# Performance work log

Hardware: AMD Instinct MI355X
Metric: run time of the kernel (lower is better)

The kernel has to match this reference:

```python
import jax, jax.numpy as jnp
import numpy as np

N = 512        # number of evidences
D = 512        # hidden_dim

def setup_inputs() -> dict:
    key = jax.random.key(0)
    k0, k1, k2, k3, k4 = jax.random.split(key, 5)
    s = 1.0 / np.sqrt(2 * D)
    return {
        "h_e":  jax.random.normal(k0, (N, D), dtype=jnp.float32),
        "W0_w": jax.random.uniform(k1, (D, 2 * D), minval=-s, maxval=s, dtype=jnp.float32),  # nn.Linear(2d, d).weight
        "W0_b": jax.random.uniform(k2, (D,), minval=-s, maxval=s, dtype=jnp.float32),
        "W1_w": jax.random.uniform(k3, (1, D), minval=-1/np.sqrt(D), maxval=1/np.sqrt(D), dtype=jnp.float32),
        "W1_b": jax.random.uniform(k4, (1,), minval=-1/np.sqrt(D), maxval=1/np.sqrt(D), dtype=jnp.float32),
    }

def reference(h_e, W0_w, W0_b, W0b_unused=None, W1_w=None, W1_b=None):
    pass  # placeholder replaced below

def reference(h_e, W0_w, W0_b, W1_w, W1_b):
    d = h_e.shape[-1]
    # W_0([h_i ; h_j]) == h_i @ A^T + h_j @ B^T where W0_w = [A | B]
    Wa = W0_w[:, :d]          # [d, d] acts on h_i
    Wb = W0_w[:, d:]          # [d, d] acts on h_j
    pre_i = jnp.einsum('id,hd->ih', h_e, Wa)            # [n, d]
    pre_j = jnp.einsum('jd,hd->jh', h_e, Wb)            # [n, d]
    hidden = jax.nn.relu(pre_i[:, None, :] + pre_j[None, :, :] + W0_b)  # [n, n, d]
    p = jnp.einsum('ijh,oh->ijo', hidden, W1_w)[..., 0] + W1_b[0]       # [n, n]
    a = jax.nn.softmax(p, axis=-1)                                      # [n, n]
    return a @ h_e                                                      # [n, d]
```

## Files before the change

kernel.cpp:

```cpp
#include <hip/hip_runtime.h>


#define LDS_STRIDE 68

using bf16x8 = __attribute__((ext_vector_type(8))) short;
using f32x4  = __attribute__((ext_vector_type(4))) float;

__device__ __forceinline__ unsigned short f2bf(float x) {
    unsigned int u = __float_as_uint(x);
    u += 0x7fffu + ((u >> 16) & 1u);
    return (unsigned short)(u >> 16);
}

__global__ __launch_bounds__(256) void k_prep(const float* __restrict__ he,
                                              const float* __restrict__ w0,
                                              unsigned short* __restrict__ heb,
                                              unsigned short* __restrict__ hebT,
                                              unsigned short* __restrict__ w0b) {
    const int tid = threadIdx.x;
    if (blockIdx.z == 0) {
        __shared__ unsigned short T[64][65];
        const int r0 = blockIdx.y * 64, c0 = blockIdx.x * 64;
        #pragma unroll
        for (int rep = 0; rep < 4; ++rep) {
            int f = tid + rep * 256;
            int row = f >> 4, col = (f & 15) * 4;
            float4 a = *(const float4*)&he[(r0 + row) * 512 + c0 + col];
            unsigned short q0 = f2bf(a.x), q1 = f2bf(a.y), q2 = f2bf(a.z), q3 = f2bf(a.w);
            *(ushort4*)&heb[(r0 + row) * 512 + c0 + col] = make_ushort4(q0, q1, q2, q3);
            T[row][col + 0] = q0; T[row][col + 1] = q1;
            T[row][col + 2] = q2; T[row][col + 3] = q3;
        }
        __syncthreads();
        #pragma unroll
        for (int rep = 0; rep < 4; ++rep) {
            int f = tid + rep * 256;
            int trow = f >> 4, tcol = (f & 15) * 4;
            ushort4 v = make_ushort4(T[tcol + 0][trow], T[tcol + 1][trow],
                                     T[tcol + 2][trow], T[tcol + 3][trow]);
            *(ushort4*)&hebT[(c0 + trow) * 512 + r0 + tcol] = v;
        }
    } else {
        const int r0 = blockIdx.y * 64, c0 = blockIdx.x * 64 + (blockIdx.z - 1) * 512;
        #pragma unroll
        for (int rep = 0; rep < 4; ++rep) {
            int f = tid + rep * 256;
            int row = f >> 4, col = (f & 15) * 4;
            float4 a = *(const float4*)&w0[(r0 + row) * 1024 + c0 + col];
            *(ushort4*)&w0b[(r0 + row) * 1024 + c0 + col] =
                make_ushort4(f2bf(a.x), f2bf(a.y), f2bf(a.z), f2bf(a.w));
        }
    }
}

__global__ __launch_bounds__(64) void k_preA(const unsigned short* __restrict__ heb,
                                             const unsigned short* __restrict__ w0b,
                                             float* __restrict__ Cfull) {
    const int l = threadIdx.x;
    const int c0 = blockIdx.x * 32;
    const int i0 = blockIdx.y * 32;
    const int r16 = l & 15;
    const int k0l = (l >> 4) * 8;
    const int hrow0 = c0 & 511;
    const int dofs = (c0 >= 512) ? 512 : 0;

    f32x4 acc[2][2] = {};
    const unsigned short* pa0 = heb + (i0 + r16) * 512;
    const unsigned short* pa1 = heb + (i0 + 16 + r16) * 512;
    const unsigned short* pb0 = w0b + (hrow0 + r16) * 1024 + dofs;
    const unsigned short* pb1 = w0b + (hrow0 + 16 + r16) * 1024 + dofs;

    #pragma unroll
    for (int ks = 0; ks < 16; ++ks) {
        const int k0 = ks * 32 + k0l;
        bf16x8 a0 = *(const bf16x8*)(pa0 + k0);
        bf16x8 a1 = *(const bf16x8*)(pa1 + k0);
        bf16x8 b0 = *(const bf16x8*)(pb0 + k0);
        bf16x8 b1 = *(const bf16x8*)(pb1 + k0);
        acc[0][0] = __builtin_amdgcn_mfma_f32_16x16x32_bf16(a0, b0, acc[0][0], 0, 0, 0);
        acc[0][1] = __builtin_amdgcn_mfma_f32_16x16x32_bf16(a0, b1, acc[0][1], 0, 0, 0);
        acc[1][0] = __builtin_amdgcn_mfma_f32_16x16x32_bf16(a1, b0, acc[1][0], 0, 0, 0);
        acc[1][1] = __builtin_amdgcn_mfma_f32_16x16x32_bf16(a1, b1, acc[1][1], 0, 0, 0);
    }
    const int orow = (l >> 4) * 4;
    #pragma unroll
    for (int ti = 0; ti < 2; ++ti)
        #pragma unroll
        for (int tj = 0; tj < 2; ++tj)
            #pragma unroll
            for (int r = 0; r < 4; ++r)
                Cfull[(i0 + ti * 16 + orow + r) * 1024 + c0 + tj * 16 + r16] = acc[ti][tj][r];
}

__global__ __launch_bounds__(256) void k_score(const float* __restrict__ Cfull,
                                               const float* __restrict__ b0,
                                               const float* __restrict__ w1,
                                               float* __restrict__ Ppart) {
    const int tid = threadIdx.x;
    const int tx = tid & 15, ty = tid >> 4;
    const int j0 = blockIdx.x * 64;
    const int i0 = blockIdx.y * 64;
    const int hs = blockIdx.z;

    __shared__ float As[32 * LDS_STRIDE];
    __shared__ float Bs[32 * LDS_STRIDE];
    __shared__ float Ws[32];

    float acc[4][4] = {};

    for (int kt = 0; kt < 2; ++kt) {
        const int hb = hs * 64 + kt * 32;
        #pragma unroll
        for (int r = 0; r < 2; ++r) {
            int f = tid + r * 256;
            int row = f >> 3;
            int hc = (f & 7) * 4;
            float4 a = *(const float4*)&Cfull[(i0 + row) * 1024 + hb + hc];
            As[(hc + 0) * LDS_STRIDE + row] = a.x;
            As[(hc + 1) * LDS_STRIDE + row] = a.y;
            As[(hc + 2) * LDS_STRIDE + row] = a.z;
            As[(hc + 3) * LDS_STRIDE + row] = a.w;
        }
        #pragma unroll
        for (int r = 0; r < 2; ++r) {
            int f = tid + r * 256;
            int row = f >> 3;
            int hc = (f & 7) * 4;
            float4 a = *(const float4*)&Cfull[(j0 + row) * 1024 + 512 + hb + hc];
            float4 bb = *(const float4*)&b0[hb + hc];
            Bs[(hc + 0) * LDS_STRIDE + row] = a.x + bb.x;
            Bs[(hc + 1) * LDS_STRIDE + row] = a.y + bb.y;
            Bs[(hc + 2) * LDS_STRIDE + row] = a.z + bb.z;
            Bs[(hc + 3) * LDS_STRIDE + row] = a.w + bb.w;
        }
        if (tid < 32) Ws[tid] = w1[hb + tid];
        __syncthreads();
        #pragma unroll
        for (int k = 0; k < 32; ++k) {
            const float4 a = *(const float4*)&As[k * LDS_STRIDE + 4 * ty];
            const float4 b = *(const float4*)&Bs[k * LDS_STRIDE + 4 * tx];
            const float w = Ws[k];
            const float av[4] = {a.x, a.y, a.z, a.w};
            const float bv[4] = {b.x, b.y, b.z, b.w};
            #pragma unroll
            for (int ii = 0; ii < 4; ++ii)
                #pragma unroll
                for (int jj = 0; jj < 4; ++jj)
                    acc[ii][jj] = fmaf(fmaxf(av[ii] + bv[jj], 0.0f), w, acc[ii][jj]);
        }
        __syncthreads();
    }
    float* outp = Ppart + (size_t)hs * 512 * 512;
    #pragma unroll
    for (int ii = 0; ii < 4; ++ii) {
        float4 v = make_float4(acc[ii][0], acc[ii][1], acc[ii][2], acc[ii][3]);
        *(float4*)&outp[(i0 + 4 * ty + ii) * 512 + j0 + 4 * tx] = v;
    }
}

__global__ __launch_bounds__(256) void k_softmax(const float* __restrict__ Ppart,
                                                 unsigned short* __restrict__ Awb) {
    const int i = blockIdx.x;
    const int tid = threadIdx.x;
    float p0 = 0.f, p1 = 0.f;
    #pragma unroll
    for (int s = 0; s < 8; ++s) {
        p0 += Ppart[s * 262144 + i * 512 + tid];
        p1 += Ppart[s * 262144 + i * 512 + tid + 256];
    }
    __shared__ float red[256];
    red[tid] = fmaxf(p0, p1);
    __syncthreads();
    for (int s = 128; s > 0; s >>= 1) {
        if (tid < s) red[tid] = fmaxf(red[tid], red[tid + s]);
        __syncthreads();
    }
    const float m = red[0];
    __syncthreads();
    const float e0 = __expf(p0 - m);
    const float e1 = __expf(p1 - m);
    red[tid] = e0 + e1;
    __syncthreads();
    for (int s = 128; s > 0; s >>= 1) {
        if (tid < s) red[tid] += red[tid + s];
        __syncthreads();
    }
    const float inv = 1.0f / red[0];
    Awb[i * 512 + tid] = f2bf(e0 * inv);
    Awb[i * 512 + tid + 256] = f2bf(e1 * inv);
}

__global__ __launch_bounds__(64) void k_outM(const unsigned short* __restrict__ Awb,
                                             const unsigned short* __restrict__ hebT,
                                             float* __restrict__ outp) {
    const int l = threadIdx.x;
    const int d0 = blockIdx.x * 32;
    const int i0 = blockIdx.y * 16;
    const int r16 = l & 15;
    const int k0l = (l >> 4) * 8;

    f32x4 acc[2] = {};
    const unsigned short* pa  = Awb  + (i0 + r16) * 512;
    const unsigned short* pb0 = hebT + (d0 + r16) * 512;
    const unsigned short* pb1 = hebT + (d0 + 16 + r16) * 512;

    #pragma unroll
    for (int ks = 0; ks < 16; ++ks) {
        const int k0 = ks * 32 + k0l;
        bf16x8 a  = *(const bf16x8*)(pa + k0);
        bf16x8 b0 = *(const bf16x8*)(pb0 + k0);
        bf16x8 b1 = *(const bf16x8*)(pb1 + k0);
        acc[0] = __builtin_amdgcn_mfma_f32_16x16x32_bf16(a, b0, acc[0], 0, 0, 0);
        acc[1] = __builtin_amdgcn_mfma_f32_16x16x32_bf16(a, b1, acc[1], 0, 0, 0);
    }
    const int orow = (l >> 4) * 4;
    #pragma unroll
    for (int tj = 0; tj < 2; ++tj)
        #pragma unroll
        for (int r = 0; r < 4; ++r)
            outp[(i0 + orow + r) * 512 + d0 + tj * 16 + r16] = acc[tj][r];
}

extern "C" void kernel_launch(void* const* d_in, const int* in_sizes, int n_in,
                              void* d_out, int out_size, void* d_ws, size_t ws_size,
                              hipStream_t stream) {
    const float* he = (const float*)d_in[0];
    const float* w0 = (const float*)d_in[1];
    const float* b0 = (const float*)d_in[2];
    const float* w1 = (const float*)d_in[3];
    float* outp = (float*)d_out;

    float* Cfull = (float*)d_ws;
    float* Ppart = Cfull + 512 * 1024;
    unsigned short* heb  = (unsigned short*)(Ppart + 8 * 512 * 512);
    unsigned short* hebT = heb + 512 * 512;
    unsigned short* w0b  = hebT + 512 * 512;
    unsigned short* Awb  = w0b + 512 * 1024;

    k_prep   <<<dim3(8, 8, 3), 256, 0, stream>>>(he, w0, heb, hebT, w0b);
    k_preA   <<<dim3(32, 16),  64,  0, stream>>>(heb, w0b, Cfull);
    k_score  <<<dim3(8, 8, 8), 256, 0, stream>>>(Cfull, b0, w1, Ppart);
    k_softmax<<<dim3(512),     256, 0, stream>>>(Ppart, Awb);
    k_outM   <<<dim3(16, 32),  64,  0, stream>>>(Awb, hebT, outp);
}
```

Measured before the change: 94.61 us.

## Use packed fp16 add/max/dot2 in score kernel and fold bias into GEMM epilogue

The precompute GEMM now writes its two projections as fp16 into separate compact arrays, adding the bias to the j-side projection in the epilogue. The pairwise score kernel loads these fp16 values, stores them as packed half2 in LDS, and computes relu(a+b) with packed fp16 add/max, then accumulates the w1 weighting with fdot2 into fp32. This halves memory and LDS traffic and roughly halves the ALU instruction count of the dominant n*n*d inner loop. The cost is fp16 rounding of the pre-activations and weights, which reduces the accuracy of the scores.

```diff
diff --git a/kernel.cpp b/kernel.cpp
--- a/kernel.cpp
+++ b/kernel.cpp
@@ -1,10 +1,12 @@
 #include <hip/hip_runtime.h>
 
-
-#define LDS_STRIDE 68
 
 using bf16x8 = __attribute__((ext_vector_type(8))) short;
 using f32x4  = __attribute__((ext_vector_type(4))) float;
+using f16x2  = __attribute__((ext_vector_type(2))) _Float16;
+using f16x8  = __attribute__((ext_vector_type(8))) _Float16;
+
+#define SC_STR 68
 
 __device__ __forceinline__ unsigned short f2bf(float x) {
     unsigned int u = __float_as_uint(x);
@@ -55,7 +57,9 @@
 
 __global__ __launch_bounds__(64) void k_preA(const unsigned short* __restrict__ heb,
                                              const unsigned short* __restrict__ w0b,
-                                             float* __restrict__ Cfull) {
+                                             const float* __restrict__ b0,
+                                             _Float16* __restrict__ CI,
+                                             _Float16* __restrict__ CJ) {
     const int l = threadIdx.x;
     const int c0 = blockIdx.x * 32;
     const int i0 = blockIdx.y * 32;
@@ -75,25 +79,41 @@
         const int k0 = ks * 32 + k0l;
         bf16x8 a0 = *(const bf16x8*)(pa0 + k0);
         bf16x8 a1 = *(const bf16x8*)(pa1 + k0);
-        bf16x8 b0 = *(const bf16x8*)(pb0 + k0);
-        bf16x8 b1 = *(const bf16x8*)(pb1 + k0);
-        acc[0][0] = __builtin_amdgcn_mfma_f32_16x16x32_bf16(a0, b0, acc[0][0], 0, 0, 0);
-        acc[0][1] = __builtin_amdgcn_mfma_f32_16x16x32_bf16(a0, b1, acc[0][1], 0, 0, 0);
-        acc[1][0] = __builtin_amdgcn_mfma_f32_16x16x32_bf16(a1, b0, acc[1][0], 0, 0, 0);
-        acc[1][1] = __builtin_amdgcn_mfma_f32_16x16x32_bf16(a1, b1, acc[1][1], 0, 0, 0);
+        bf16x8 b0v = *(const bf16x8*)(pb0 + k0);
+        bf16x8 b1v = *(const bf16x8*)(pb1 + k0);
+        acc[0][0] = __builtin_amdgcn_mfma_f32_16x16x32_bf16(a0, b0v, acc[0][0], 0, 0, 0);
+        acc[0][1] = __builtin_amdgcn_mfma_f32_16x16x32_bf16(a0, b1v, acc[0][1], 0, 0, 0);
+        acc[1][0] = __builtin_amdgcn_mfma_f32_16x16x32_bf16(a1, b0v, acc[1][0], 0, 0, 0);
+        acc[1][1] = __builtin_amdgcn_mfma_f32_16x16x32_bf16(a1, b1v, acc[1][1], 0, 0, 0);
     }
     const int orow = (l >> 4) * 4;
-    #pragma unroll
-    for (int ti = 0; ti < 2; ++ti)
-        #pragma unroll
-        for (int tj = 0; tj < 2; ++tj)
+    if (dofs) {
+        const float bb0 = b0[hrow0 + r16];
+        const float bb1 = b0[hrow0 + 16 + r16];
+        #pragma unroll
+        for (int ti = 0; ti < 2; ++ti)
             #pragma unroll
-            for (int r = 0; r < 4; ++r)
-                Cfull[(i0 + ti * 16 + orow + r) * 1024 + c0 + tj * 16 + r16] = acc[ti][tj][r];
-}
-
-__global__ __launch_bounds__(256) void k_score(const float* __restrict__ Cfull,
-                                               const float* __restrict__ b0,
+            for (int tj = 0; tj < 2; ++tj) {
+                const float bb = tj ? bb1 : bb0;
+                #pragma unroll
+                for (int r = 0; r < 4; ++r)
+                    CJ[(i0 + ti * 16 + orow + r) * 512 + hrow0 + tj * 16 + r16] =
+                        (_Float16)(acc[ti][tj][r] + bb);
+            }
+    } else {
+        #pragma unroll
+        for (int ti = 0; ti < 2; ++ti)
+            #pragma unroll
+            for (int tj = 0; tj < 2; ++tj)
+                #pragma unroll
+                for (int r = 0; r < 4; ++r)
+                    CI[(i0 + ti * 16 + orow + r) * 512 + c0 + tj * 16 + r16] =
+                        (_Float16)acc[ti][tj][r];
+    }
+}
+
+__global__ __launch_bounds__(256) void k_score(const _Float16* __restrict__ CI,
+                                               const _Float16* __restrict__ CJ,
                                                const float* __restrict__ w1,
                                                float* __restrict__ Ppart) {
     const int tid = threadIdx.x;
@@ -102,51 +122,57 @@
     const int i0 = blockIdx.y * 64;
     const int hs = blockIdx.z;
 
-    __shared__ float As[32 * LDS_STRIDE];
-    __shared__ float Bs[32 * LDS_STRIDE];
-    __shared__ float Ws[32];
-
+    __shared__ __align__(16) f16x2 As2[16 * SC_STR];
+    __shared__ __align__(16) f16x2 Bs2[16 * SC_STR];
+    __shared__ f16x2 Ws2[16];
+
+    const f16x2 fz = {(_Float16)0, (_Float16)0};
     float acc[4][4] = {};
 
     for (int kt = 0; kt < 2; ++kt) {
         const int hb = hs * 64 + kt * 32;
-        #pragma unroll
-        for (int r = 0; r < 2; ++r) {
-            int f = tid + r * 256;
-            int row = f >> 3;
-            int hc = (f & 7) * 4;
-            float4 a = *(const float4*)&Cfull[(i0 + row) * 1024 + hb + hc];
-            As[(hc + 0) * LDS_STRIDE + row] = a.x;
-            As[(hc + 1) * LDS_STRIDE + row] = a.y;
-            As[(hc + 2) * LDS_STRIDE + row] = a.z;
-            As[(hc + 3) * LDS_STRIDE + row] = a.w;
-        }
-        #pragma unroll
-        for (int r = 0; r < 2; ++r) {
-            int f = tid + r * 256;
-            int row = f >> 3;
-            int hc = (f & 7) * 4;
-            float4 a = *(const float4*)&Cfull[(j0 + row) * 1024 + 512 + hb + hc];
-            float4 bb = *(const float4*)&b0[hb + hc];
-            Bs[(hc + 0) * LDS_STRIDE + row] = a.x + bb.x;
-            Bs[(hc + 1) * LDS_STRIDE + row] = a.y + bb.y;
-            Bs[(hc + 2) * LDS_STRIDE + row] = a.z + bb.z;
-            Bs[(hc + 3) * LDS_STRIDE + row] = a.w + bb.w;
-        }
-        if (tid < 32) Ws[tid] = w1[hb + tid];
-        __syncthreads();
-        #pragma unroll
-        for (int k = 0; k < 32; ++k) {
-            const float4 a = *(const float4*)&As[k * LDS_STRIDE + 4 * ty];
-            const float4 b = *(const float4*)&Bs[k * LDS_STRIDE + 4 * tx];
-            const float w = Ws[k];
-            const float av[4] = {a.x, a.y, a.z, a.w};
-            const float bv[4] = {b.x, b.y, b.z, b.w};
+        {
+            const int row = tid >> 2;
+            const int hc = (tid & 3) * 8;
+            const int hp = hc >> 1;
+            f16x8 av = *(const f16x8*)&CI[(i0 + row) * 512 + hb + hc];
+            As2[(hp + 0) * SC_STR + row] = __builtin_shufflevector(av, av, 0, 1);
+            As2[(hp + 1) * SC_STR + row] = __builtin_shufflevector(av, av, 2, 3);
+            As2[(hp + 2) * SC_STR + row] = __builtin_shufflevector(av, av, 4, 5);
+            As2[(hp + 3) * SC_STR + row] = __builtin_shufflevector(av, av, 6, 7);
+            f16x8 bv = *(const f16x8*)&CJ[(j0 + row) * 512 + hb + hc];
+            Bs2[(hp + 0) * SC_STR + row] = __builtin_shufflevector(bv, bv, 0, 1);
+            Bs2[(hp + 1) * SC_STR + row] = __builtin_shufflevector(bv, bv, 2, 3);
+            Bs2[(hp + 2) * SC_STR + row] = __builtin_shufflevector(bv, bv, 4, 5);
+            Bs2[(hp + 3) * SC_STR + row] = __builtin_shufflevector(bv, bv, 6, 7);
+        }
+        if (tid < 16) {
+            float2 w = *(const float2*)&w1[hb + 2 * tid];
+            f16x2 wp = {(_Float16)w.x, (_Float16)w.y};
+            Ws2[tid] = wp;
+        }
+        __syncthreads();
+        #pragma unroll
+        for (int k = 0; k < 16; ++k) {
+            f16x8 a8 = *(const f16x8*)&As2[k * SC_STR + 4 * ty];
+            f16x8 b8 = *(const f16x8*)&Bs2[k * SC_STR + 4 * tx];
+            const f16x2 w = Ws2[k];
+            f16x2 ap[4] = { __builtin_shufflevector(a8, a8, 0, 1),
+                            __builtin_shufflevector(a8, a8, 2, 3),
+                            __builtin_shufflevector(a8, a8, 4, 5),
+                            __builtin_shufflevector(a8, a8, 6, 7) };
+            f16x2 bp[4] = { __builtin_shufflevector(b8, b8, 0, 1),
+                            __builtin_shufflevector(b8, b8, 2, 3),
+                            __builtin_shufflevector(b8, b8, 4, 5),
+                            __builtin_shufflevector(b8, b8, 6, 7) };
             #pragma unroll
             for (int ii = 0; ii < 4; ++ii)
                 #pragma unroll
-                for (int jj = 0; jj < 4; ++jj)
-                    acc[ii][jj] = fmaf(fmaxf(av[ii] + bv[jj], 0.0f), w, acc[ii][jj]);
+                for (int jj = 0; jj < 4; ++jj) {
+                    f16x2 s = ap[ii] + bp[jj];
+                    s = __builtin_elementwise_max(s, fz);
+                    acc[ii][jj] = __builtin_amdgcn_fdot2(s, w, acc[ii][jj], false);
+                }
         }
         __syncthreads();
     }
@@ -230,16 +256,17 @@
     const float* w1 = (const float*)d_in[3];
     float* outp = (float*)d_out;
 
-    float* Cfull = (float*)d_ws;
-    float* Ppart = Cfull + 512 * 1024;
-    unsigned short* heb  = (unsigned short*)(Ppart + 8 * 512 * 512);
+    float* Ppart = (float*)d_ws;
+    _Float16* CI = (_Float16*)(Ppart + 8 * 512 * 512);
+    _Float16* CJ = CI + 512 * 512;
+    unsigned short* heb  = (unsigned short*)(CJ + 512 * 512);
     unsigned short* hebT = heb + 512 * 512;
     unsigned short* w0b  = hebT + 512 * 512;
     unsigned short* Awb  = w0b + 512 * 1024;
 
     k_prep   <<<dim3(8, 8, 3), 256, 0, stream>>>(he, w0, heb, hebT, w0b);
-    k_preA   <<<dim3(32, 16),  64,  0, stream>>>(heb, w0b, Cfull);
-    k_score  <<<dim3(8, 8, 8), 256, 0, stream>>>(Cfull, b0, w1, Ppart);
+    k_preA   <<<dim3(32, 16),  64,  0, stream>>>(heb, w0b, b0, CI, CJ);
+    k_score  <<<dim3(8, 8, 8), 256, 0, stream>>>(CI, CJ, w1, Ppart);
     k_softmax<<<dim3(512),     256, 0, stream>>>(Ppart, Awb);
     k_outM   <<<dim3(16, 32),  64,  0, stream>>>(Awb, hebT, outp);
 }
```

Measured after the change: 91.89 us. -2.9%, faster.
